# Performance work log

Measured on AMD Instinct MI355X. Metric: run time of the kernel, lower is better.

The kernel has to match this reference:

```python
import jax, jax.numpy as jnp
import numpy as np

N_V = 2          # n_v from init
LN_EPS = 1e-5    # torch nn.LayerNorm default


def _layernorm(x, gamma, beta):
    # LayerNorm over last dim (dim_in)
    mu = jnp.mean(x, axis=-1, keepdims=True)
    var = jnp.var(x, axis=-1, keepdims=True)
    return (x - mu) * jax.lax.rsqrt(var + LN_EPS) * gamma + beta


def setup_inputs() -> dict:
    key = jax.random.key(0)
    k0, k1, k2, k3, k4 = jax.random.split(key, 5)
    E, D, N = 160000, 128, 10000
    return {
        "edge_index": jax.random.randint(k0, (E, 2), 0, N, dtype=jnp.int32),
        "vec": jax.random.normal(k1, (E, 3, D), dtype=jnp.float32),
        "pos_vec1": jax.random.normal(k2, (N_V, E, D), dtype=jnp.float32),
        "pos_vec2": jax.random.normal(k3, (N_V, E, D), dtype=jnp.float32),
        "edge_vec": jax.random.normal(k4, (E, 3), dtype=jnp.float32),
        "ln_gamma": jnp.ones((D,), dtype=jnp.float32),
        "ln_beta": jnp.zeros((D,), dtype=jnp.float32),
    }


def reference(edge_index, vec, pos_vec1, pos_vec2, edge_vec, ln_gamma, ln_beta):
    # propagate_v2 with last_layer=False
    ei = edge_index.T                     # [2, E]
    E, _, D = vec.shape
    nnode = E                             # source: nnode = vec.shape[0]
    # message: [E,3,D]; source always uses list index 0
    msg = vec * pos_vec1[0][:, None, :] + pos_vec2[0][:, None, :] * edge_vec[:, :, None]
    # aggregate: scatter-add over target index, then collect (gather) back to edges
    agg = jax.ops.segment_sum(msg.reshape(E, 3 * D), ei[1], num_segments=nnode)
    lifted = agg[ei[0]].reshape(E, 3, D)  # __collect__ via source index (flow=source_to_target)
    normed = _layernorm(lifted, ln_gamma, ln_beta)
    # the n_v loop recomputes the identical result (indexes [0] each time)
    return jnp.stack([normed] * N_V, axis=0)  # [n_v, E, 3, D]
```

## Files before the change

kernel.cpp:

```cpp
#include <hip/hip_runtime.h>

#define D 128
#define NNODE 10000
#define LN_EPS 1e-5f

typedef float v4f __attribute__((ext_vector_type(4)));

__global__ __launch_bounds__(256) void hist_kernel(
    const int* __restrict__ ei, int* __restrict__ cnt, int E)
{
    int e = blockIdx.x * 256 + threadIdx.x;
    if (e < E) atomicAdd(&cnt[ei[2 * e + 1]], 1);
}

#define SCAN_T 1024
#define CHUNK 10
__global__ __launch_bounds__(SCAN_T) void scan_kernel(
    const int* __restrict__ cnt, int* __restrict__ offs, int* __restrict__ cur)
{
    __shared__ int sums[SCAN_T];
    int t = threadIdx.x;
    int base = t * CHUNK;
    int local[CHUNK];
    int s = 0;
#pragma unroll
    for (int i = 0; i < CHUNK; ++i) {
        int idx = base + i;
        int v = (idx < NNODE) ? cnt[idx] : 0;
        local[i] = v; s += v;
    }
    sums[t] = s;
    __syncthreads();
    for (int off = 1; off < SCAN_T; off <<= 1) {
        int v = 0;
        if (t >= off) v = sums[t - off];
        __syncthreads();
        sums[t] += v;
        __syncthreads();
    }
    int run = (t > 0) ? sums[t - 1] : 0;
#pragma unroll
    for (int i = 0; i < CHUNK; ++i) {
        int idx = base + i;
        if (idx < NNODE) { offs[idx] = run; cur[idx] = run; run += local[i]; }
    }
    if (t == SCAN_T - 1) offs[NNODE] = sums[SCAN_T - 1];
}

__global__ __launch_bounds__(256) void fill_kernel(
    const int* __restrict__ ei, int* __restrict__ cur, int* __restrict__ csr, int E)
{
    int e = blockIdx.x * 256 + threadIdx.x;
    if (e < E) {
        int pos = atomicAdd(&cur[ei[2 * e + 1]], 1);
        csr[pos] = e;
    }
}

__global__ __launch_bounds__(256) void aggregate_kernel(
    const int* __restrict__ offs, const int* __restrict__ csr,
    const float4* __restrict__ vec4,
    const float4* __restrict__ pv14,
    const float4* __restrict__ pv24,
    const float* __restrict__ edge_vec,
    float4* __restrict__ agg4)
{
    int n = blockIdx.x * 8 + (threadIdx.x >> 5);
    int j = threadIdx.x & 31;
    if (n >= NNODE) return;
    int beg = offs[n], end = offs[n + 1];
    float4 a0 = {0, 0, 0, 0}, a1 = {0, 0, 0, 0}, a2 = {0, 0, 0, 0};
    for (int k0 = beg; k0 < end; k0 += 32) {
        int nk = end - k0;
        if (nk > 32) nk = 32;
        int eid = (k0 + j < end) ? csr[k0 + j] : 0;
        for (int t = 0; t < nk; ++t) {
            int e = __shfl(eid, t, 32);
            float4 p1 = pv14[e * 32 + j];
            float4 p2 = pv24[e * 32 + j];
            float e0 = edge_vec[e * 3 + 0];
            float e1 = edge_vec[e * 3 + 1];
            float e2 = edge_vec[e * 3 + 2];
            float4 v0 = vec4[(e * 3 + 0) * 32 + j];
            float4 v1 = vec4[(e * 3 + 1) * 32 + j];
            float4 v2 = vec4[(e * 3 + 2) * 32 + j];
            a0.x = fmaf(v0.x, p1.x, fmaf(p2.x, e0, a0.x));
            a0.y = fmaf(v0.y, p1.y, fmaf(p2.y, e0, a0.y));
            a0.z = fmaf(v0.z, p1.z, fmaf(p2.z, e0, a0.z));
            a0.w = fmaf(v0.w, p1.w, fmaf(p2.w, e0, a0.w));
            a1.x = fmaf(v1.x, p1.x, fmaf(p2.x, e1, a1.x));
            a1.y = fmaf(v1.y, p1.y, fmaf(p2.y, e1, a1.y));
            a1.z = fmaf(v1.z, p1.z, fmaf(p2.z, e1, a1.z));
            a1.w = fmaf(v1.w, p1.w, fmaf(p2.w, e1, a1.w));
            a2.x = fmaf(v2.x, p1.x, fmaf(p2.x, e2, a2.x));
            a2.y = fmaf(v2.y, p1.y, fmaf(p2.y, e2, a2.y));
            a2.z = fmaf(v2.z, p1.z, fmaf(p2.z, e2, a2.z));
            a2.w = fmaf(v2.w, p1.w, fmaf(p2.w, e2, a2.w));
        }
    }
    agg4[(n * 3 + 0) * 32 + j] = a0;
    agg4[(n * 3 + 1) * 32 + j] = a1;
    agg4[(n * 3 + 2) * 32 + j] = a2;
}

__global__ __launch_bounds__(256) void mpnn_gather_ln(
    const int* __restrict__ edge_index,
    const float* __restrict__ agg,
    const float4* __restrict__ gamma4,
    const float4* __restrict__ beta4,
    float* __restrict__ out,
    long long copy_stride,
    int n_copy,
    int nrows)
{
    int row = blockIdx.x * 8 + (threadIdx.x >> 5);
    int l = threadIdx.x & 31;
    if (row >= nrows) return;
    int e = row / 3;
    int c = row - e * 3;
    int src = edge_index[e * 2];

    float4 x = *(const float4*)(agg + ((long long)src * 3 + c) * D + l * 4);

    float s = x.x + x.y + x.z + x.w;
#pragma unroll
    for (int off = 16; off > 0; off >>= 1) s += __shfl_xor(s, off);
    float mu = s * (1.0f / (float)D);

    float dx = x.x - mu, dy = x.y - mu, dz = x.z - mu, dw = x.w - mu;
    float sq = dx * dx + dy * dy + dz * dz + dw * dw;
#pragma unroll
    for (int off = 16; off > 0; off >>= 1) sq += __shfl_xor(sq, off);
    float rstd = rsqrtf(sq * (1.0f / (float)D) + LN_EPS);

    float4 g = gamma4[l];
    float4 b = beta4[l];
    v4f y;
    y.x = fmaf(dx * rstd, g.x, b.x);
    y.y = fmaf(dy * rstd, g.y, b.y);
    y.z = fmaf(dz * rstd, g.z, b.z);
    y.w = fmaf(dw * rstd, g.w, b.w);

    long long o = (long long)row * D + l * 4;
#pragma unroll 2
    for (int k = 0; k < n_copy; ++k)
        __builtin_nontemporal_store(y, (v4f*)(out + (long long)k * copy_stride + o));
}

extern "C" void kernel_launch(void* const* d_in, const int* in_sizes, int n_in,
                              void* d_out, int out_size, void* d_ws, size_t ws_size,
                              hipStream_t stream) {
    const int*   edge_index = (const int*)d_in[0];
    const float* vec        = (const float*)d_in[1];
    const float* pv1        = (const float*)d_in[2];
    const float* pv2        = (const float*)d_in[3];
    const float* edge_vec   = (const float*)d_in[4];
    const float* gamma      = (const float*)d_in[5];
    const float* beta       = (const float*)d_in[6];
    float* out = (float*)d_out;

    int E = in_sizes[4] / 3;
    long long copy_stride = (long long)E * 3 * D;
    int n_copy = (int)((long long)out_size / copy_stride);

    size_t agg_bytes  = (size_t)NNODE * 3 * D * sizeof(float);
    size_t cnt_bytes  = (size_t)NNODE * sizeof(int);
    size_t offs_bytes = (size_t)(NNODE + 1) * sizeof(int);
    size_t cur_bytes  = (size_t)NNODE * sizeof(int);
    size_t csr_bytes  = (size_t)E * sizeof(int);
    size_t need = agg_bytes + cnt_bytes + offs_bytes + cur_bytes + csr_bytes + 64;

    bool use_ws = (ws_size >= need);
    char* base;
    if (use_ws) {
        base = (char*)d_ws;
    } else {
        uintptr_t endp = (uintptr_t)((char*)d_out + (size_t)out_size * sizeof(float));
        base = (char*)((endp - need) & ~(uintptr_t)15);
    }
    float* agg  = (float*)base;
    int*   cnt  = (int*)(base + agg_bytes);
    int*   offs = (int*)(base + agg_bytes + cnt_bytes);
    int*   cur  = (int*)(base + agg_bytes + cnt_bytes + offs_bytes);
    int*   csr  = (int*)(base + agg_bytes + cnt_bytes + offs_bytes + cur_bytes);

    hipMemsetAsync(cnt, 0, cnt_bytes, stream);

    int eb = (E + 255) / 256;
    hist_kernel<<<eb, 256, 0, stream>>>(edge_index, cnt, E);
    scan_kernel<<<1, SCAN_T, 0, stream>>>(cnt, offs, cur);
    fill_kernel<<<eb, 256, 0, stream>>>(edge_index, cur, csr, E);
    aggregate_kernel<<<(NNODE + 7) / 8, 256, 0, stream>>>(
        offs, csr, (const float4*)vec, (const float4*)pv1,
        (const float4*)pv2, edge_vec, (float4*)agg);

    int nrows = E * 3;
    int blocks = (nrows + 7) / 8;
    if (use_ws) {
        mpnn_gather_ln<<<blocks, 256, 0, stream>>>(
            edge_index, agg, (const float4*)gamma, (const float4*)beta,
            out, copy_stride, n_copy, nrows);
    } else {
        mpnn_gather_ln<<<blocks, 256, 0, stream>>>(
            edge_index, agg, (const float4*)gamma, (const float4*)beta,
            out, copy_stride, 1, nrows);
        for (int k = 1; k < n_copy; ++k)
            hipMemcpyAsync(out + (long long)k * copy_stride, out,
                           copy_stride * sizeof(float),
                           hipMemcpyDeviceToDevice, stream);
    }
}
```

Measured before the change: 246.2 us.

## Fuse LayerNorm into node aggregation and broadcast normalized rows to edges

LayerNorm now runs once per node inside the aggregation kernel, which is valid because the gathered rows depend only on the source node. The per-edge kernel becomes a pure gather-and-store of the already normalized rows, so the 480k-row reduction work shrinks to 30k rows. When no workspace is available, the scratch buffer lives in the tail of the output. Instead of issuing memcpy calls for the extra copies, the broadcast kernel skips the tail rows of the last copy and a fixup kernel fills them afterwards.

```diff
diff --git a/kernel.cpp b/kernel.cpp
--- a/kernel.cpp
+++ b/kernel.cpp
@@ -57,13 +57,15 @@
     }
 }
 
-__global__ __launch_bounds__(256) void aggregate_kernel(
+__global__ __launch_bounds__(256) void aggregate_ln_kernel(
     const int* __restrict__ offs, const int* __restrict__ csr,
     const float4* __restrict__ vec4,
     const float4* __restrict__ pv14,
     const float4* __restrict__ pv24,
     const float* __restrict__ edge_vec,
-    float4* __restrict__ agg4)
+    const float4* __restrict__ gamma4,
+    const float4* __restrict__ beta4,
+    float4* __restrict__ normed4)
 {
     int n = blockIdx.x * 8 + (threadIdx.x >> 5);
     int j = threadIdx.x & 31;
@@ -98,19 +100,35 @@
             a2.w = fmaf(v2.w, p1.w, fmaf(p2.w, e2, a2.w));
         }
     }
-    agg4[(n * 3 + 0) * 32 + j] = a0;
-    agg4[(n * 3 + 1) * 32 + j] = a1;
-    agg4[(n * 3 + 2) * 32 + j] = a2;
-}
-
-__global__ __launch_bounds__(256) void mpnn_gather_ln(
+    float4 g = gamma4[j], b = beta4[j];
+#pragma unroll
+    for (int c = 0; c < 3; ++c) {
+        float4 a = (c == 0) ? a0 : ((c == 1) ? a1 : a2);
+        float s = a.x + a.y + a.z + a.w;
+#pragma unroll
+        for (int off = 16; off > 0; off >>= 1) s += __shfl_xor(s, off);
+        float mu = s * (1.0f / (float)D);
+        float dx = a.x - mu, dy = a.y - mu, dz = a.z - mu, dw = a.w - mu;
+        float sq = dx * dx + dy * dy + dz * dz + dw * dw;
+#pragma unroll
+        for (int off = 16; off > 0; off >>= 1) sq += __shfl_xor(sq, off);
+        float rstd = rsqrtf(sq * (1.0f / (float)D) + LN_EPS);
+        float4 y;
+        y.x = fmaf(dx * rstd, g.x, b.x);
+        y.y = fmaf(dy * rstd, g.y, b.y);
+        y.z = fmaf(dz * rstd, g.z, b.z);
+        y.w = fmaf(dw * rstd, g.w, b.w);
+        normed4[(n * 3 + c) * 32 + j] = y;
+    }
+}
+
+__global__ __launch_bounds__(256) void broadcast_kernel(
     const int* __restrict__ edge_index,
-    const float* __restrict__ agg,
-    const float4* __restrict__ gamma4,
-    const float4* __restrict__ beta4,
+    const float4* __restrict__ normed4,
     float* __restrict__ out,
     long long copy_stride,
     int n_copy,
+    int skip_row,
     int nrows)
 {
     int row = blockIdx.x * 8 + (threadIdx.x >> 5);
@@ -119,32 +137,22 @@
     int e = row / 3;
     int c = row - e * 3;
     int src = edge_index[e * 2];
-
-    float4 x = *(const float4*)(agg + ((long long)src * 3 + c) * D + l * 4);
-
-    float s = x.x + x.y + x.z + x.w;
-#pragma unroll
-    for (int off = 16; off > 0; off >>= 1) s += __shfl_xor(s, off);
-    float mu = s * (1.0f / (float)D);
-
-    float dx = x.x - mu, dy = x.y - mu, dz = x.z - mu, dw = x.w - mu;
-    float sq = dx * dx + dy * dy + dz * dz + dw * dw;
-#pragma unroll
-    for (int off = 16; off > 0; off >>= 1) sq += __shfl_xor(sq, off);
-    float rstd = rsqrtf(sq * (1.0f / (float)D) + LN_EPS);
-
-    float4 g = gamma4[l];
-    float4 b = beta4[l];
-    v4f y;
-    y.x = fmaf(dx * rstd, g.x, b.x);
-    y.y = fmaf(dy * rstd, g.y, b.y);
-    y.z = fmaf(dz * rstd, g.z, b.z);
-    y.w = fmaf(dw * rstd, g.w, b.w);
-
+    v4f y = *(const v4f*)(normed4 + ((long long)src * 3 + c) * 32 + l);
     long long o = (long long)row * D + l * 4;
-#pragma unroll 2
-    for (int k = 0; k < n_copy; ++k)
+    for (int k = 0; k < n_copy; ++k) {
+        if (k == n_copy - 1 && row >= skip_row) break;
         __builtin_nontemporal_store(y, (v4f*)(out + (long long)k * copy_stride + o));
+    }
+}
+
+__global__ __launch_bounds__(256) void fixup_kernel(
+    float* __restrict__ out, long long copy_stride, int n_copy,
+    long long start4, long long n4)
+{
+    long long i = (long long)blockIdx.x * 256 + threadIdx.x;
+    if (i >= n4) return;
+    v4f y = *(const v4f*)(out + (start4 + i) * 4);
+    *(v4f*)(out + (long long)(n_copy - 1) * copy_stride + (start4 + i) * 4) = y;
 }
 
 extern "C" void kernel_launch(void* const* d_in, const int* in_sizes, int n_in,
@@ -162,51 +170,54 @@
     int E = in_sizes[4] / 3;
     long long copy_stride = (long long)E * 3 * D;
     int n_copy = (int)((long long)out_size / copy_stride);
-
-    size_t agg_bytes  = (size_t)NNODE * 3 * D * sizeof(float);
+    int nrows = E * 3;
+
+    size_t normed_bytes = (size_t)NNODE * 3 * D * sizeof(float);
     size_t cnt_bytes  = (size_t)NNODE * sizeof(int);
     size_t offs_bytes = (size_t)(NNODE + 1) * sizeof(int);
     size_t cur_bytes  = (size_t)NNODE * sizeof(int);
     size_t csr_bytes  = (size_t)E * sizeof(int);
-    size_t need = agg_bytes + cnt_bytes + offs_bytes + cur_bytes + csr_bytes + 64;
+    size_t need = normed_bytes + cnt_bytes + offs_bytes + cur_bytes + csr_bytes + 256;
 
     bool use_ws = (ws_size >= need);
     char* base;
+    int skip_row = nrows;
     if (use_ws) {
         base = (char*)d_ws;
     } else {
-        uintptr_t endp = (uintptr_t)((char*)d_out + (size_t)out_size * sizeof(float));
-        base = (char*)((endp - need) & ~(uintptr_t)15);
-    }
-    float* agg  = (float*)base;
-    int*   cnt  = (int*)(base + agg_bytes);
-    int*   offs = (int*)(base + agg_bytes + cnt_bytes);
-    int*   cur  = (int*)(base + agg_bytes + cnt_bytes + offs_bytes);
-    int*   csr  = (int*)(base + agg_bytes + cnt_bytes + offs_bytes + cur_bytes);
-
-    hipMemsetAsync(cnt, 0, cnt_bytes, stream);
+        uintptr_t endp = (uintptr_t)(out + (size_t)out_size);
+        base = (char*)((endp - need) & ~(uintptr_t)255);
+        long long base_off = (long long)((char*)base - (char*)out);
+        long long rel = base_off - (long long)(n_copy - 1) * copy_stride * 4;
+        skip_row = (int)(rel / (D * 4));
+        if (skip_row > nrows) skip_row = nrows;
+        if (skip_row < 0) skip_row = 0;
+    }
+    float* normed = (float*)base;
+    int*   cnt  = (int*)(base + normed_bytes);
+    int*   offs = (int*)(base + normed_bytes + cnt_bytes);
+    int*   cur  = (int*)(base + normed_bytes + cnt_bytes + offs_bytes);
+    int*   csr  = (int*)(base + normed_bytes + cnt_bytes + offs_bytes + cur_bytes);
+
+    (void)hipMemsetAsync(cnt, 0, cnt_bytes, stream);
 
     int eb = (E + 255) / 256;
     hist_kernel<<<eb, 256, 0, stream>>>(edge_index, cnt, E);
     scan_kernel<<<1, SCAN_T, 0, stream>>>(cnt, offs, cur);
     fill_kernel<<<eb, 256, 0, stream>>>(edge_index, cur, csr, E);
-    aggregate_kernel<<<(NNODE + 7) / 8, 256, 0, stream>>>(
+    aggregate_ln_kernel<<<(NNODE + 7) / 8, 256, 0, stream>>>(
         offs, csr, (const float4*)vec, (const float4*)pv1,
-        (const float4*)pv2, edge_vec, (float4*)agg);
-
-    int nrows = E * 3;
-    int blocks = (nrows + 7) / 8;
-    if (use_ws) {
-        mpnn_gather_ln<<<blocks, 256, 0, stream>>>(
-            edge_index, agg, (const float4*)gamma, (const float4*)beta,
-            out, copy_stride, n_copy, nrows);
-    } else {
-        mpnn_gather_ln<<<blocks, 256, 0, stream>>>(
-            edge_index, agg, (const float4*)gamma, (const float4*)beta,
-            out, copy_stride, 1, nrows);
-        for (int k = 1; k < n_copy; ++k)
-            hipMemcpyAsync(out + (long long)k * copy_stride, out,
-                           copy_stride * sizeof(float),
-                           hipMemcpyDeviceToDevice, stream);
-    }
-}
+        (const float4*)pv2, edge_vec,
+        (const float4*)gamma, (const float4*)beta, (float4*)normed);
+
+    broadcast_kernel<<<(nrows + 7) / 8, 256, 0, stream>>>(
+        edge_index, (const float4*)normed, out, copy_stride, n_copy,
+        skip_row, nrows);
+
+    if (skip_row < nrows) {
+        long long start4 = (long long)skip_row * (D / 4);
+        long long n4 = (long long)nrows * (D / 4) - start4;
+        int fb = (int)((n4 + 255) / 256);
+        fixup_kernel<<<fb, 256, 0, stream>>>(out, copy_stride, n_copy, start4, n4);
+    }
+}
```

After: 233.7 us. -5.1%, faster.
